# Kernel tuning notes

Measured on AMD Instinct MI355X. Metric: run time of the kernel, lower is better.

Reference implementation:

```python
import jax, jax.numpy as jnp
import numpy as np

DIM = 512
EPS = 1e-08
N_LAYERS = 3


def setup_inputs() -> dict:
    key = jax.random.key(0)
    ks = jax.random.split(key, 1 + 2 * N_LAYERS)
    B, N1 = 4, 2049  # batch, tokens (1 cls + 2048 feat)
    x = jax.random.normal(ks[0], (B, N1, DIM), dtype=jnp.float32)
    inp = {"x": x}
    s = 1.0 / np.sqrt(DIM)
    for i in range(N_LAYERS):
        inp[f"W{i}"] = jax.random.uniform(ks[1 + 2 * i], (DIM, DIM), jnp.float32, -s, s)
        inp[f"b{i}"] = jax.random.uniform(ks[2 + 2 * i], (DIM,), jnp.float32, -s, s)
    return inp


def _pgcn(x, Ws, bs):
    cls_token = x[:, 0]          # [B, D]
    feat = x[:, 1:]              # [B, N, D]
    n = jnp.linalg.norm(feat, axis=2, keepdims=True)
    feat_norm = feat / jnp.maximum(n, EPS)
    sim = jnp.einsum('bnd,bmd->bnm', feat_norm, feat_norm)  # [B, N, N]
    N = sim.shape[1]
    topk = max(int(N * 0.01), 100)
    # torch.topk(largest=False): kth-smallest value per row is the threshold
    kth_smallest = -jax.lax.top_k(-sim, topk)[0][..., -1:]  # [B, N, 1]
    adj = jnp.where(sim >= kth_smallest, sim, 0.0)
    # 3-layer GCN (skip_connection=False, eval mode -> dropout is identity)
    h = feat
    for W, b in zip(Ws, bs):
        support = jnp.einsum('bnd,de->bne', h, W) + b
        h = jax.nn.relu(jnp.einsum('bnm,bmd->bnd', adj, support))
    return jnp.concatenate([cls_token[:, None, :], h], axis=1)


def reference(x, W0, b0, W1, b1, W2, b2):
    return _pgcn(x, (W0, W1, W2), (b0, b1, b2))
```

## Files before the change

kernel.cpp:

```cpp
#include <hip/hip_runtime.h>
#include <hip/hip_bf16.h>
#include <math.h>

#define DIMV   512
#define NTOK   2048
#define NROWS  2049
#define NB     4
#define KSEL   100
#define EPSV   1e-8f

typedef __bf16 bf16x8 __attribute__((ext_vector_type(8)));
typedef float  f32x4  __attribute__((ext_vector_type(4)));

__device__ __forceinline__ unsigned short f2bf(float f) {
  unsigned int u = __float_as_uint(f);
  u += 0x7fffu + ((u >> 16) & 1u);
  return (unsigned short)(u >> 16);
}
__device__ __forceinline__ float bf2f(unsigned short s) {
  return __uint_as_float(((unsigned int)s) << 16);
}

#define GLDS16(g, l)                                                         \
  __builtin_amdgcn_global_load_lds(                                          \
      (const __attribute__((address_space(1))) void*)(unsigned long long)(g),\
      (__attribute__((address_space(3))) void*)(unsigned int)(unsigned long long)(l), \
      16, 0, 0)

__global__ __launch_bounds__(256) void normalize_kernel(const float* __restrict__ x,
                                                        unsigned short* __restrict__ fhi,
                                                        unsigned short* __restrict__ flo,
                                                        unsigned short* __restrict__ featb) {
  const int wave = blockIdx.x * 4 + (threadIdx.x >> 6);
  const int lane = threadIdx.x & 63;
  const int b = wave / NTOK, r = wave % NTOK;
  const float* src = x + (long)(b * NROWS + 1 + r) * DIMV;
  const long rowoff = (long)(b * NTOK + r) * DIMV;
  float4 v0 = reinterpret_cast<const float4*>(src)[lane];
  float4 v1 = reinterpret_cast<const float4*>(src)[lane + 64];
  ushort4 u0, u1;
  u0.x = f2bf(v0.x); u0.y = f2bf(v0.y); u0.z = f2bf(v0.z); u0.w = f2bf(v0.w);
  u1.x = f2bf(v1.x); u1.y = f2bf(v1.y); u1.z = f2bf(v1.z); u1.w = f2bf(v1.w);
  reinterpret_cast<ushort4*>(featb + rowoff)[lane] = u0;
  reinterpret_cast<ushort4*>(featb + rowoff)[lane + 64] = u1;
  float ss = v0.x*v0.x + v0.y*v0.y + v0.z*v0.z + v0.w*v0.w
           + v1.x*v1.x + v1.y*v1.y + v1.z*v1.z + v1.w*v1.w;
  #pragma unroll
  for (int m = 1; m < 64; m <<= 1) ss += __shfl_xor(ss, m, 64);
  const float scale = 1.0f / fmaxf(sqrtf(ss), EPSV);
  float f[8] = {v0.x*scale, v0.y*scale, v0.z*scale, v0.w*scale,
                v1.x*scale, v1.y*scale, v1.z*scale, v1.w*scale};
  ushort4 h0, h1, l0, l1;
  unsigned short hh[8], ll[8];
  #pragma unroll
  for (int i = 0; i < 8; i++) {
    hh[i] = f2bf(f[i]);
    ll[i] = f2bf(f[i] - bf2f(hh[i]));
  }
  h0.x = hh[0]; h0.y = hh[1]; h0.z = hh[2]; h0.w = hh[3];
  h1.x = hh[4]; h1.y = hh[5]; h1.z = hh[6]; h1.w = hh[7];
  l0.x = ll[0]; l0.y = ll[1]; l0.z = ll[2]; l0.w = ll[3];
  l1.x = ll[4]; l1.y = ll[5]; l1.z = ll[6]; l1.w = ll[7];
  reinterpret_cast<ushort4*>(fhi + rowoff)[lane]      = h0;
  reinterpret_cast<ushort4*>(fhi + rowoff)[lane + 64] = h1;
  reinterpret_cast<ushort4*>(flo + rowoff)[lane]      = l0;
  reinterpret_cast<ushort4*>(flo + rowoff)[lane + 64] = l1;
}

__global__ __launch_bounds__(256)
void sim_split_kernel(const unsigned short* __restrict__ Fhi,
                      const unsigned short* __restrict__ Flo,
                      float* __restrict__ C)
{
  __shared__ unsigned short AsH[128 * 32];
  __shared__ unsigned short AsL[128 * 32];
  __shared__ unsigned short BsH[128 * 32];
  __shared__ unsigned short BsL[128 * 32];
  const int t = threadIdx.x;
  const int l = t & 63;
  const int w = t >> 6;
  const int wr = w >> 1, wc = w & 1;
  const int zb = blockIdx.z;
  const int ti = blockIdx.x;
  int by = (int)((sqrtf(8.0f * (float)ti + 1.0f) - 1.0f) * 0.5f);
  while ((by + 1) * (by + 2) / 2 <= ti) by++;
  while (by * (by + 1) / 2 > ti) by--;
  const int bx = ti - by * (by + 1) / 2;
  const unsigned short* Ahi = Fhi + (long)zb * NTOK * DIMV;
  const unsigned short* Alo = Flo + (long)zb * NTOK * DIMV;
  const int row0 = by * 128;
  const int col0 = bx * 128;

  f32x4 acc[4][4];
  #pragma unroll
  for (int m = 0; m < 4; m++)
    #pragma unroll
    for (int n = 0; n < 4; n++) acc[m][n] = (f32x4){0.f, 0.f, 0.f, 0.f};

  const int r0 = t >> 2;
  const int r1 = 64 + (t >> 2);
  const int part = t & 3;
  const size_t base0 = (size_t)((t & 192) * 8);
  const size_t base1 = (size_t)((256 + (t & 192)) * 8);
  const int fr = l & 15, fg = l >> 4;

  for (int k0 = 0; k0 < DIMV; k0 += 32) {
    GLDS16(Ahi + (long)(row0 + r0) * DIMV + k0 + part * 8, AsH + base0);
    GLDS16(Ahi + (long)(row0 + r1) * DIMV + k0 + part * 8, AsH + base1);
    GLDS16(Alo + (long)(row0 + r0) * DIMV + k0 + part * 8, AsL + base0);
    GLDS16(Alo + (long)(row0 + r1) * DIMV + k0 + part * 8, AsL + base1);
    GLDS16(Ahi + (long)(col0 + r0) * DIMV + k0 + part * 8, BsH + base0);
    GLDS16(Ahi + (long)(col0 + r1) * DIMV + k0 + part * 8, BsH + base1);
    GLDS16(Alo + (long)(col0 + r0) * DIMV + k0 + part * 8, BsL + base0);
    GLDS16(Alo + (long)(col0 + r1) * DIMV + k0 + part * 8, BsL + base1);
    __syncthreads();

    bf16x8 ah[4], al[4], bh[4], bl[4];
    #pragma unroll
    for (int m = 0; m < 4; m++) {
      const int off = (wr * 64 + m * 16 + fr) * 32 + fg * 8;
      ah[m] = *reinterpret_cast<const bf16x8*>(&AsH[off]);
      al[m] = *reinterpret_cast<const bf16x8*>(&AsL[off]);
    }
    #pragma unroll
    for (int n = 0; n < 4; n++) {
      const int off = (wc * 64 + n * 16 + fr) * 32 + fg * 8;
      bh[n] = *reinterpret_cast<const bf16x8*>(&BsH[off]);
      bl[n] = *reinterpret_cast<const bf16x8*>(&BsL[off]);
    }
    #pragma unroll
    for (int m = 0; m < 4; m++)
      #pragma unroll
      for (int n = 0; n < 4; n++) {
        acc[m][n] = __builtin_amdgcn_mfma_f32_16x16x32_bf16(ah[m], bh[n], acc[m][n], 0, 0, 0);
        acc[m][n] = __builtin_amdgcn_mfma_f32_16x16x32_bf16(ah[m], bl[n], acc[m][n], 0, 0, 0);
        acc[m][n] = __builtin_amdgcn_mfma_f32_16x16x32_bf16(al[m], bh[n], acc[m][n], 0, 0, 0);
      }
    __syncthreads();
  }

  float* Cb = C + (long)zb * NTOK * NTOK;
  #pragma unroll
  for (int m = 0; m < 4; m++)
    #pragma unroll
    for (int r = 0; r < 4; r++) {
      const int row = row0 + wr * 64 + m * 16 + fg * 4 + r;
      #pragma unroll
      for (int n = 0; n < 4; n++) {
        const int col = col0 + wc * 64 + n * 16 + fr;
        Cb[(long)row * NTOK + col] = acc[m][n][r];
      }
    }
  if (bx != by) {
    #pragma unroll
    for (int m = 0; m < 4; m++)
      #pragma unroll
      for (int r = 0; r < 4; r++) {
        const int row = row0 + wr * 64 + m * 16 + fg * 4 + r;
        #pragma unroll
        for (int n = 0; n < 4; n++) {
          const int col = col0 + wc * 64 + n * 16 + fr;
          Cb[(long)col * NTOK + row] = acc[m][n][r];
        }
      }
  }
}

template<bool BIAS, bool RELU, bool BF16OUT>
__global__ __launch_bounds__(256)
void mfma_gemm(const unsigned short* __restrict__ A,
               const unsigned short* __restrict__ Bt,
               const float* __restrict__ bias,
               void* __restrict__ Cv,
               int K, int lda, int ldb, int ldc,
               long sA, long sB, long sC)
{
  __shared__ unsigned short As[128 * 32];
  __shared__ unsigned short Bs[64 * 32];
  const int t = threadIdx.x;
  const int l = t & 63;
  const int w = t >> 6;
  const int wr = w >> 1, wc = w & 1;
  const int zb = blockIdx.z;
  A  += (long)zb * sA;
  Bt += (long)zb * sB;
  const int row0 = blockIdx.y * 128;
  const int col0 = blockIdx.x * 64;

  f32x4 acc[4][2];
  #pragma unroll
  for (int m = 0; m < 4; m++)
    #pragma unroll
    for (int n = 0; n < 2; n++) acc[m][n] = (f32x4){0.f, 0.f, 0.f, 0.f};

  const int arow0 = t >> 2;
  const int arow1 = (t + 256) >> 2;
  const int apart = t & 3;
  const int brow  = t >> 2, bpart = t & 3;
  unsigned short* ldsA0 = As + (size_t)((t & 192) * 8);
  unsigned short* ldsA1 = As + (size_t)((256 + (t & 192)) * 8);
  unsigned short* ldsB  = Bs + (size_t)((t & 192) * 8);
  const int fr = l & 15, fg = l >> 4;

  const int nk = K >> 5;
  for (int kk = 0; kk < nk; ++kk) {
    const int k0 = kk << 5;
    GLDS16(A  + (long)(row0 + arow0) * lda + k0 + apart * 8, ldsA0);
    GLDS16(A  + (long)(row0 + arow1) * lda + k0 + apart * 8, ldsA1);
    GLDS16(Bt + (long)(col0 + brow)  * ldb + k0 + bpart * 8, ldsB);
    __syncthreads();

    bf16x8 af[4], bfr[2];
    #pragma unroll
    for (int m = 0; m < 4; m++)
      af[m] = *reinterpret_cast<const bf16x8*>(
          &As[(wr * 64 + m * 16 + fr) * 32 + fg * 8]);
    #pragma unroll
    for (int n = 0; n < 2; n++)
      bfr[n] = *reinterpret_cast<const bf16x8*>(
          &Bs[(wc * 32 + n * 16 + fr) * 32 + fg * 8]);
    #pragma unroll
    for (int m = 0; m < 4; m++)
      #pragma unroll
      for (int n = 0; n < 2; n++)
        acc[m][n] = __builtin_amdgcn_mfma_f32_16x16x32_bf16(af[m], bfr[n],
                                                            acc[m][n], 0, 0, 0);
    __syncthreads();
  }

  #pragma unroll
  for (int m = 0; m < 4; m++) {
    #pragma unroll
    for (int r = 0; r < 4; r++) {
      const int row = row0 + wr * 64 + m * 16 + fg * 4 + r;
      float bv = 0.f;
      if (BIAS) bv = bias[row];
      #pragma unroll
      for (int n = 0; n < 2; n++) {
        const int col = col0 + wc * 32 + n * 16 + fr;
        float v = acc[m][n][r] + bv;
        if (RELU) v = fmaxf(v, 0.f);
        if (BF16OUT)
          ((unsigned short*)Cv)[(long)zb * sC + (long)row * ldc + col] = f2bf(v);
        else
          ((float*)Cv)[(long)zb * sC + (long)row * ldc + col] = v;
      }
    }
  }
}

__global__ __launch_bounds__(256) void kthmask_kernel(const float* __restrict__ sim,
                                                      unsigned short* __restrict__ adjb) {
  const int wid = blockIdx.x * 4 + (threadIdx.x >> 6);
  const int lane = threadIdx.x & 63;
  const float4* row = reinterpret_cast<const float4*>(sim + (long)wid * NTOK);
  unsigned int key[32];
  #pragma unroll
  for (int i = 0; i < 8; i++) {
    const float4 v = row[lane + i * 64];
    const float f[4] = {v.x, v.y, v.z, v.w};
    #pragma unroll
    for (int j = 0; j < 4; j++) {
      const unsigned int b = __float_as_uint(f[j]);
      key[i * 4 + j] = (b & 0x80000000u) ? ~b : (b | 0x80000000u);
    }
  }
  unsigned int lo = 0u, hi = 0xFFFFFFFFu;
  for (int it = 0; it < 32; ++it) {
    const unsigned int mid =
        (unsigned int)(((unsigned long long)lo + (unsigned long long)hi) >> 1);
    unsigned int total = 0;
    #pragma unroll
    for (int j = 0; j < 32; j++)
      total += (unsigned int)__popcll(__ballot(key[j] <= mid));
    if (total >= KSEL) hi = mid; else lo = mid + 1u;
  }
  ushort4* orow = reinterpret_cast<ushort4*>(adjb + (long)wid * NTOK);
  #pragma unroll
  for (int i = 0; i < 8; i++) {
    ushort4 o;
    unsigned short* op = &o.x;
    #pragma unroll
    for (int j = 0; j < 4; j++) {
      const unsigned int k = key[i * 4 + j];
      const unsigned int bits = (k & 0x80000000u) ? (k ^ 0x80000000u) : ~k;
      op[j] = (k >= lo) ? f2bf(__uint_as_float(bits)) : (unsigned short)0;
    }
    orow[lane + i * 64] = o;
  }
}

__global__ __launch_bounds__(256) void wcast_kernel(const float* __restrict__ W,
                                                    unsigned short* __restrict__ WT) {
  __shared__ float tile[32][33];
  const int tx = threadIdx.x & 31, ty = threadIdx.x >> 5;
  const int bx = blockIdx.x, by = blockIdx.y;
  #pragma unroll
  for (int s = 0; s < 32; s += 8)
    tile[ty + s][tx] = W[(long)(by * 32 + ty + s) * DIMV + bx * 32 + tx];
  __syncthreads();
  #pragma unroll
  for (int s = 0; s < 32; s += 8)
    WT[(long)(bx * 32 + ty + s) * DIMV + by * 32 + tx] = f2bf(tile[tx][ty + s]);
}

__global__ void cls_copy(const float* __restrict__ x, float* __restrict__ out) {
  const int b = blockIdx.x;
  out[(long)b * NROWS * DIMV + threadIdx.x] = x[(long)b * NROWS * DIMV + threadIdx.x];
}

extern "C" void kernel_launch(void* const* d_in, const int* in_sizes, int n_in,
                              void* d_out, int out_size, void* d_ws, size_t ws_size,
                              hipStream_t stream) {
  const float* x  = (const float*)d_in[0];
  const float* Ws[3] = {(const float*)d_in[1], (const float*)d_in[3], (const float*)d_in[5]};
  const float* bs[3] = {(const float*)d_in[2], (const float*)d_in[4], (const float*)d_in[6]};
  float* out = (float*)d_out;

  char* ws = (char*)d_ws;
  unsigned short* fhi    = (unsigned short*)(ws);
  unsigned short* flo    = (unsigned short*)(ws + 8388608UL);
  float*          sim    = (float*)(ws + 16777216UL);
  unsigned short* adjb   = (unsigned short*)(ws + 83886080UL);
  unsigned short* supT   = (unsigned short*)(ws + 117440512UL);
  unsigned short* hb     = (unsigned short*)(ws + 125829120UL);
  unsigned short* wtb    = (unsigned short*)(ws + 134217728UL);

  normalize_kernel<<<dim3(NB * NTOK / 4), 256, 0, stream>>>(x, fhi, flo, hb);

  for (int lyr = 0; lyr < 3; lyr++)
    wcast_kernel<<<dim3(16, 16), 256, 0, stream>>>(Ws[lyr], wtb + (long)lyr * DIMV * DIMV);

  sim_split_kernel<<<dim3(136, 1, NB), 256, 0, stream>>>(fhi, flo, sim);

  kthmask_kernel<<<dim3(NB * NTOK / 4), 256, 0, stream>>>(sim, adjb);

  for (int lyr = 0; lyr < 3; lyr++) {
    mfma_gemm<true, false, true>
        <<<dim3(NTOK/64, DIMV/128, NB), 256, 0, stream>>>(
        wtb + (long)lyr * DIMV * DIMV, hb, bs[lyr], supT,
        DIMV, DIMV, DIMV, NTOK,
        0L, (long)NTOK * DIMV, (long)DIMV * NTOK);
    if (lyr < 2) {
      mfma_gemm<false, true, true>
          <<<dim3(DIMV/64, NTOK/128, NB), 256, 0, stream>>>(
          adjb, supT, nullptr, hb,
          NTOK, NTOK, NTOK, DIMV,
          (long)NTOK * NTOK, (long)DIMV * NTOK, (long)NTOK * DIMV);
    } else {
      mfma_gemm<false, true, false>
          <<<dim3(DIMV/64, NTOK/128, NB), 256, 0, stream>>>(
          adjb, supT, nullptr, out + DIMV,
          NTOK, NTOK, NTOK, DIMV,
          (long)NTOK * NTOK, (long)DIMV * NTOK, (long)NROWS * DIMV);
    }
  }

  cls_copy<<<dim3(NB), DIMV, 0, stream>>>(x, out);
}
```

Baseline: 280.8 us.

## Merge prep launches, fuse layer-0 support GEMM into kth-mask kernel, remap GEMM blocks

The three weight-cast launches and the cls copy become one prep kernel with a z-indexed grid. The first layer's support GEMM now runs as extra blocks in the same launch as the kth-smallest masking, so the two independent stages can overlap and one launch is removed. The standalone GEMM gets a block-index remap that strides linear block IDs across groups of eight. The aim is lower launch overhead and better GPU fill, at the cost of mixing heterogeneous blocks in one launch, which may hurt occupancy or leave some blocks waiting.

```diff
diff --git a/kernel.cpp b/kernel.cpp
--- a/kernel.cpp
+++ b/kernel.cpp
@@ -65,6 +65,35 @@
   reinterpret_cast<ushort4*>(fhi + rowoff)[lane + 64] = h1;
   reinterpret_cast<ushort4*>(flo + rowoff)[lane]      = l0;
   reinterpret_cast<ushort4*>(flo + rowoff)[lane + 64] = l1;
+}
+
+__global__ __launch_bounds__(256) void prep_kernel(const float* __restrict__ W0,
+                                                   const float* __restrict__ W1,
+                                                   const float* __restrict__ W2,
+                                                   unsigned short* __restrict__ WT,
+                                                   const float* __restrict__ x,
+                                                   float* __restrict__ out) {
+  const int z = blockIdx.z;
+  if (z == 3) {
+    if (blockIdx.y == 0 && blockIdx.x < 8) {
+      const int b = blockIdx.x >> 1, half = blockIdx.x & 1;
+      const long off = (long)b * NROWS * DIMV + half * 256 + threadIdx.x;
+      out[off] = x[off];
+    }
+    return;
+  }
+  const float* W = (z == 0) ? W0 : (z == 1) ? W1 : W2;
+  unsigned short* WTl = WT + (long)z * DIMV * DIMV;
+  __shared__ float tile[32][33];
+  const int tx = threadIdx.x & 31, ty = threadIdx.x >> 5;
+  const int bx = blockIdx.x, by = blockIdx.y;
+  #pragma unroll
+  for (int s = 0; s < 32; s += 8)
+    tile[ty + s][tx] = W[(long)(by * 32 + ty + s) * DIMV + bx * 32 + tx];
+  __syncthreads();
+  #pragma unroll
+  for (int s = 0; s < 32; s += 8)
+    WTl[(long)(bx * 32 + ty + s) * DIMV + by * 32 + tx] = f2bf(tile[tx][ty + s]);
 }
 
 __global__ __launch_bounds__(256)
@@ -167,6 +196,88 @@
 }
 
 template<bool BIAS, bool RELU, bool BF16OUT>
+__device__ __forceinline__
+void gemm_body(const unsigned short* __restrict__ A,
+               const unsigned short* __restrict__ Bt,
+               const float* __restrict__ bias,
+               void* __restrict__ Cv,
+               int K, int lda, int ldb, int ldc,
+               long sA, long sB, long sC,
+               int bx, int by, int bz,
+               unsigned short* As, unsigned short* Bs)
+{
+  const int t = threadIdx.x;
+  const int l = t & 63;
+  const int w = t >> 6;
+  const int wr = w >> 1, wc = w & 1;
+  A  += (long)bz * sA;
+  Bt += (long)bz * sB;
+  const int row0 = by * 128;
+  const int col0 = bx * 64;
+
+  f32x4 acc[4][2];
+  #pragma unroll
+  for (int m = 0; m < 4; m++)
+    #pragma unroll
+    for (int n = 0; n < 2; n++) acc[m][n] = (f32x4){0.f, 0.f, 0.f, 0.f};
+
+  const int arow0 = t >> 2;
+  const int arow1 = (t + 256) >> 2;
+  const int apart = t & 3;
+  const int brow  = t >> 2, bpart = t & 3;
+  unsigned short* ldsA0 = As + (size_t)((t & 192) * 8);
+  unsigned short* ldsA1 = As + (size_t)((256 + (t & 192)) * 8);
+  unsigned short* ldsB  = Bs + (size_t)((t & 192) * 8);
+  const int fr = l & 15, fg = l >> 4;
+
+  const int nk = K >> 5;
+  for (int kk = 0; kk < nk; ++kk) {
+    const int k0 = kk << 5;
+    GLDS16(A  + (long)(row0 + arow0) * lda + k0 + apart * 8, ldsA0);
+    GLDS16(A  + (long)(row0 + arow1) * lda + k0 + apart * 8, ldsA1);
+    GLDS16(Bt + (long)(col0 + brow)  * ldb + k0 + bpart * 8, ldsB);
+    __syncthreads();
+
+    bf16x8 af[4], bfr[2];
+    #pragma unroll
+    for (int m = 0; m < 4; m++)
+      af[m] = *reinterpret_cast<const bf16x8*>(
+          &As[(wr * 64 + m * 16 + fr) * 32 + fg * 8]);
+    #pragma unroll
+    for (int n = 0; n < 2; n++)
+      bfr[n] = *reinterpret_cast<const bf16x8*>(
+          &Bs[(wc * 32 + n * 16 + fr) * 32 + fg * 8]);
+    #pragma unroll
+    for (int m = 0; m < 4; m++)
+      #pragma unroll
+      for (int n = 0; n < 2; n++)
+        acc[m][n] = __builtin_amdgcn_mfma_f32_16x16x32_bf16(af[m], bfr[n],
+                                                            acc[m][n], 0, 0, 0);
+    __syncthreads();
+  }
+
+  #pragma unroll
+  for (int m = 0; m < 4; m++) {
+    #pragma unroll
+    for (int r = 0; r < 4; r++) {
+      const int row = row0 + wr * 64 + m * 16 + fg * 4 + r;
+      float bv = 0.f;
+      if (BIAS) bv = bias[row];
+      #pragma unroll
+      for (int n = 0; n < 2; n++) {
+        const int col = col0 + wc * 32 + n * 16 + fr;
+        float v = acc[m][n][r] + bv;
+        if (RELU) v = fmaxf(v, 0.f);
+        if (BF16OUT)
+          ((unsigned short*)Cv)[(long)bz * sC + (long)row * ldc + col] = f2bf(v);
+        else
+          ((float*)Cv)[(long)bz * sC + (long)row * ldc + col] = v;
+      }
+    }
+  }
+}
+
+template<bool BIAS, bool RELU, bool BF16OUT>
 __global__ __launch_bounds__(256)
 void mfma_gemm(const unsigned short* __restrict__ A,
                const unsigned short* __restrict__ Bt,
@@ -177,80 +288,38 @@
 {
   __shared__ unsigned short As[128 * 32];
   __shared__ unsigned short Bs[64 * 32];
-  const int t = threadIdx.x;
-  const int l = t & 63;
-  const int w = t >> 6;
-  const int wr = w >> 1, wc = w & 1;
-  const int zb = blockIdx.z;
-  A  += (long)zb * sA;
-  Bt += (long)zb * sB;
-  const int row0 = blockIdx.y * 128;
-  const int col0 = blockIdx.x * 64;
-
-  f32x4 acc[4][2];
-  #pragma unroll
-  for (int m = 0; m < 4; m++)
-    #pragma unroll
-    for (int n = 0; n < 2; n++) acc[m][n] = (f32x4){0.f, 0.f, 0.f, 0.f};
-
-  const int arow0 = t >> 2;
-  const int arow1 = (t + 256) >> 2;
-  const int apart = t & 3;
-  const int brow  = t >> 2, bpart = t & 3;
-  unsigned short* ldsA0 = As + (size_t)((t & 192) * 8);
-  unsigned short* ldsA1 = As + (size_t)((256 + (t & 192)) * 8);
-  unsigned short* ldsB  = Bs + (size_t)((t & 192) * 8);
-  const int fr = l & 15, fg = l >> 4;
-
-  const int nk = K >> 5;
-  for (int kk = 0; kk < nk; ++kk) {
-    const int k0 = kk << 5;
-    GLDS16(A  + (long)(row0 + arow0) * lda + k0 + apart * 8, ldsA0);
-    GLDS16(A  + (long)(row0 + arow1) * lda + k0 + apart * 8, ldsA1);
-    GLDS16(Bt + (long)(col0 + brow)  * ldb + k0 + bpart * 8, ldsB);
-    __syncthreads();
-
-    bf16x8 af[4], bfr[2];
-    #pragma unroll
-    for (int m = 0; m < 4; m++)
-      af[m] = *reinterpret_cast<const bf16x8*>(
-          &As[(wr * 64 + m * 16 + fr) * 32 + fg * 8]);
-    #pragma unroll
-    for (int n = 0; n < 2; n++)
-      bfr[n] = *reinterpret_cast<const bf16x8*>(
-          &Bs[(wc * 32 + n * 16 + fr) * 32 + fg * 8]);
-    #pragma unroll
-    for (int m = 0; m < 4; m++)
-      #pragma unroll
-      for (int n = 0; n < 2; n++)
-        acc[m][n] = __builtin_amdgcn_mfma_f32_16x16x32_bf16(af[m], bfr[n],
-                                                            acc[m][n], 0, 0, 0);
-    __syncthreads();
-  }
-
-  #pragma unroll
-  for (int m = 0; m < 4; m++) {
-    #pragma unroll
-    for (int r = 0; r < 4; r++) {
-      const int row = row0 + wr * 64 + m * 16 + fg * 4 + r;
-      float bv = 0.f;
-      if (BIAS) bv = bias[row];
-      #pragma unroll
-      for (int n = 0; n < 2; n++) {
-        const int col = col0 + wc * 32 + n * 16 + fr;
-        float v = acc[m][n][r] + bv;
-        if (RELU) v = fmaxf(v, 0.f);
-        if (BF16OUT)
-          ((unsigned short*)Cv)[(long)zb * sC + (long)row * ldc + col] = f2bf(v);
-        else
-          ((float*)Cv)[(long)zb * sC + (long)row * ldc + col] = v;
-      }
-    }
-  }
-}
-
-__global__ __launch_bounds__(256) void kthmask_kernel(const float* __restrict__ sim,
-                                                      unsigned short* __restrict__ adjb) {
+  const int nx = gridDim.x, ny = gridDim.y;
+  int lin = blockIdx.x + nx * (blockIdx.y + ny * blockIdx.z);
+  const int nwg = nx * ny * (int)gridDim.z;
+  const int chunk = nwg >> 3;
+  lin = (lin & 7) * chunk + (lin >> 3);
+  const int bx = lin % nx;
+  const int tmp = lin / nx;
+  const int by = tmp % ny;
+  const int bz = tmp / ny;
+  gemm_body<BIAS, RELU, BF16OUT>(A, Bt, bias, Cv, K, lda, ldb, ldc,
+                                 sA, sB, sC, bx, by, bz, As, Bs);
+}
+
+__global__ __launch_bounds__(256)
+void kthgemm_kernel(const float* __restrict__ sim,
+                    unsigned short* __restrict__ adjb,
+                    const unsigned short* __restrict__ WT0,
+                    const unsigned short* __restrict__ hb,
+                    const float* __restrict__ bias0,
+                    unsigned short* __restrict__ supT)
+{
+  __shared__ unsigned short As[128 * 32];
+  __shared__ unsigned short Bs[64 * 32];
+  if (blockIdx.x >= 2048) {
+    const int bid = blockIdx.x - 2048;
+    const int bx = bid & 31, by = (bid >> 5) & 3, bz = bid >> 7;
+    gemm_body<true, false, true>(WT0, hb, bias0, supT,
+                                 DIMV, DIMV, DIMV, NTOK,
+                                 0L, (long)NTOK * DIMV, (long)DIMV * NTOK,
+                                 bx, by, bz, As, Bs);
+    return;
+  }
   const int wid = blockIdx.x * 4 + (threadIdx.x >> 6);
   const int lane = threadIdx.x & 63;
   const float4* row = reinterpret_cast<const float4*>(sim + (long)wid * NTOK);
@@ -288,25 +357,6 @@
     }
     orow[lane + i * 64] = o;
   }
-}
-
-__global__ __launch_bounds__(256) void wcast_kernel(const float* __restrict__ W,
-                                                    unsigned short* __restrict__ WT) {
-  __shared__ float tile[32][33];
-  const int tx = threadIdx.x & 31, ty = threadIdx.x >> 5;
-  const int bx = blockIdx.x, by = blockIdx.y;
-  #pragma unroll
-  for (int s = 0; s < 32; s += 8)
-    tile[ty + s][tx] = W[(long)(by * 32 + ty + s) * DIMV + bx * 32 + tx];
-  __syncthreads();
-  #pragma unroll
-  for (int s = 0; s < 32; s += 8)
-    WT[(long)(bx * 32 + ty + s) * DIMV + by * 32 + tx] = f2bf(tile[tx][ty + s]);
-}
-
-__global__ void cls_copy(const float* __restrict__ x, float* __restrict__ out) {
-  const int b = blockIdx.x;
-  out[(long)b * NROWS * DIMV + threadIdx.x] = x[(long)b * NROWS * DIMV + threadIdx.x];
 }
 
 extern "C" void kernel_launch(void* const* d_in, const int* in_sizes, int n_in,
@@ -328,19 +378,20 @@
 
   normalize_kernel<<<dim3(NB * NTOK / 4), 256, 0, stream>>>(x, fhi, flo, hb);
 
-  for (int lyr = 0; lyr < 3; lyr++)
-    wcast_kernel<<<dim3(16, 16), 256, 0, stream>>>(Ws[lyr], wtb + (long)lyr * DIMV * DIMV);
+  prep_kernel<<<dim3(16, 16, 4), 256, 0, stream>>>(Ws[0], Ws[1], Ws[2], wtb, x, out);
 
   sim_split_kernel<<<dim3(136, 1, NB), 256, 0, stream>>>(fhi, flo, sim);
 
-  kthmask_kernel<<<dim3(NB * NTOK / 4), 256, 0, stream>>>(sim, adjb);
+  kthgemm_kernel<<<dim3(2560), 256, 0, stream>>>(sim, adjb, wtb, hb, bs[0], supT);
 
   for (int lyr = 0; lyr < 3; lyr++) {
-    mfma_gemm<true, false, true>
-        <<<dim3(NTOK/64, DIMV/128, NB), 256, 0, stream>>>(
-        wtb + (long)lyr * DIMV * DIMV, hb, bs[lyr], supT,
-        DIMV, DIMV, DIMV, NTOK,
-        0L, (long)NTOK * DIMV, (long)DIMV * NTOK);
+    if (lyr > 0) {
+      mfma_gemm<true, false, true>
+          <<<dim3(NTOK/64, DIMV/128, NB), 256, 0, stream>>>(
+          wtb + (long)lyr * DIMV * DIMV, hb, bs[lyr], supT,
+          DIMV, DIMV, DIMV, NTOK,
+          0L, (long)NTOK * DIMV, (long)DIMV * NTOK);
+    }
     if (lyr < 2) {
       mfma_gemm<false, true, true>
           <<<dim3(DIMV/64, NTOK/128, NB), 256, 0, stream>>>(
@@ -355,6 +406,4 @@
           (long)NTOK * NTOK, (long)DIMV * NTOK, (long)NROWS * DIMV);
     }
   }
-
-  cls_copy<<<dim3(NB), DIMV, 0, stream>>>(x, out);
-}
+}
```

Measured after the change: 244.6 us. 1.15x faster.
